# Kernel optimization log

Hardware: AMD Instinct MI355X
Metric: run time of the kernel (lower is better)

The kernel has to match this reference:

```python
import jax, jax.numpy as jnp
import numpy as np

R, DIL = 3, 2  # radius, dilation for neighbor correlation


def conv2d(x, w, b):
    # standard 3x3 stride-1 SAME conv, NCHW / OIHW
    y = jax.lax.conv_general_dilated(x, w, (1, 1), 'SAME',
                                     dimension_numbers=('NCHW', 'OIHW', 'NCHW'))
    return y + b[None, :, None, None]


def bilinear_gather(x, py, px):
    # x: (n,c,h,w); py/px: (n,K,h,w) float sampling coords; zero outside bounds
    n, c, h, w = x.shape
    y0 = jnp.floor(py); x0 = jnp.floor(px)
    wy = py - y0; wx = px - x0
    xf = x.reshape(n, c, h * w)

    def gather(yi, xi):
        valid = ((yi >= 0) & (yi < h) & (xi >= 0) & (xi < w)).astype(x.dtype)
        yc = jnp.clip(yi, 0, h - 1).astype(jnp.int32)
        xc = jnp.clip(xi, 0, w - 1).astype(jnp.int32)
        idx = (yc * w + xc).reshape(n, -1)  # (n, K*h*w)
        v = jax.vmap(lambda f, i: f[:, i])(xf, idx)  # (n, c, K*h*w)
        return v.reshape(n, c, *yi.shape[1:]) * valid[:, None]

    v00 = gather(y0, x0); v01 = gather(y0, x0 + 1)
    v10 = gather(y0 + 1, x0); v11 = gather(y0 + 1, x0 + 1)
    wy_ = wy[:, None]; wx_ = wx[:, None]
    return (v00 * (1 - wy_) * (1 - wx_) + v01 * (1 - wy_) * wx_
            + v10 * wy_ * (1 - wx_) + v11 * wy_ * wx_)


def dcn(x, w, b, ow, ob):
    # DCNv2-style modulated deformable 3x3 conv, stride 1, pad 1, 1 deformable group.
    # Offset/mask predicted by an internal conv: channels = [dy(9), dx(9), mask(9)].
    n, c, h, w_ = x.shape
    K = 9
    om = conv2d(x, ow, ob)  # (n, 27, h, w)
    dy, dx = om[:, :K], om[:, K:2 * K]
    mask = jax.nn.sigmoid(om[:, 2 * K:])
    ky, kx = jnp.meshgrid(jnp.arange(-1, 2), jnp.arange(-1, 2), indexing='ij')
    ky = ky.reshape(K).astype(x.dtype); kx = kx.reshape(K).astype(x.dtype)
    yy = jnp.arange(h, dtype=x.dtype)[None, None, :, None]
    xx = jnp.arange(w_, dtype=x.dtype)[None, None, None, :]
    py = yy + ky[None, :, None, None] + dy  # (n,K,h,w)
    px = xx + kx[None, :, None, None] + dx
    samp = bilinear_gather(x, py, px) * mask[:, None]  # (n,c,K,h,w)
    return jnp.einsum('nckhw,ock->nohw', samp, w.reshape(w.shape[0], c, K)) + b[None, :, None, None]


def ncf(f1, f2, radius, dilation):
    # neighbor_correlation_filter: unfold-based sliding-window dot-product attention
    n, c, h, w = f2.shape
    k = 2 * radius + 1
    pad = (k - 1) * dilation // 2
    f2p = jnp.pad(f2, ((0, 0), (0, 0), (pad, pad), (pad, pad)))
    # (n,c,K,h,w), tap order (ky outer, kx inner) matching F.unfold row-major layout
    patches = jnp.stack([f2p[:, :, i * dilation:i * dilation + h, j * dilation:j * dilation + w]
                         for i in range(k) for j in range(k)], axis=2)
    corr = jnp.einsum('nchw,nckhw->nkhw', f1, patches) / jnp.sqrt(jnp.asarray(c, f1.dtype))
    attn = jax.nn.softmax(corr, axis=1)
    sample = jnp.einsum('nkhw,nckhw->nchw', attn, patches)
    return sample, corr


def stargru(x, t, zw, zb, zow, zob, hw, hb, how, hob):
    tx = jnp.concatenate([x, t], axis=1)
    z = jax.nn.sigmoid(dcn(tx, zw, zb, zow, zob))
    r, _ = ncf(t, x, R, DIL)
    xt = jnp.tanh(dcn(jnp.concatenate([r, t], axis=1), hw, hb, how, hob))
    return (1.0 - z) * t + z * xt


def setup_inputs():
    key = jax.random.key(0)
    N, CIN, CH, H, W = 2, 256, 64, 96, 96
    ks = iter(jax.random.split(key, 32))

    def rn(shape, s=0.05):
        return jax.random.normal(next(ks), shape, jnp.float32) * s

    inp = {
        'x': jax.random.normal(next(ks), (N, CIN, H, W), jnp.float32),
        'template': jax.random.normal(next(ks), (N, CH, H, W), jnp.float32),
        'w_in': rn((CH, CIN, 3, 3)), 'b_in': jnp.zeros((CH,), jnp.float32),
        'w_out': rn((CIN, CH, 3, 3)), 'b_out': jnp.zeros((CIN,), jnp.float32),
    }
    for pre in ('enh_z', 'enh_h', 'upd_z', 'upd_h'):
        inp[pre + '_w'] = rn((CH, 2 * CH, 3, 3))
        inp[pre + '_b'] = jnp.zeros((CH,), jnp.float32)
        inp[pre + '_ow'] = rn((27, 2 * CH, 3, 3), 0.01)  # offset/mask conv (small init)
        inp[pre + '_ob'] = jnp.zeros((27,), jnp.float32)
    return inp


def reference(x, template, w_in, b_in, w_out, b_out,
              enh_z_w, enh_z_b, enh_z_ow, enh_z_ob,
              enh_h_w, enh_h_b, enh_h_ow, enh_h_ob,
              upd_z_w, upd_z_b, upd_z_ow, upd_z_ob,
              upd_h_w, upd_h_b, upd_h_ow, upd_h_ob):
    # CrossUpdate forward, post-first-frame branch (self.template is not None)
    xh = conv2d(x, w_in, b_in)
    x_enh = stargru(template, xh,
                    enh_z_w, enh_z_b, enh_z_ow, enh_z_ob,
                    enh_h_w, enh_h_b, enh_h_ow, enh_h_ob)
    new_template = stargru(xh, template,
                           upd_z_w, upd_z_b, upd_z_ow, upd_z_ob,
                           upd_h_w, upd_h_b, upd_h_ow, upd_h_ob)
    out = conv2d(x_enh, w_out, b_out)
    return (out, new_template)
```

## Files before the change

kernel.cpp:

```cpp
#include <hip/hip_runtime.h>
#include <hip/hip_bf16.h>

typedef __hip_bfloat16 bf16;
typedef unsigned short u16;
typedef unsigned int u32;
typedef __attribute__((ext_vector_type(8))) short short8;
typedef __attribute__((ext_vector_type(4))) short bh4;
typedef __attribute__((ext_vector_type(4))) float floatx4;

constexpr int N_ = 2, H_ = 96, W_ = 96, HW_ = H_ * W_;
constexpr int CIN_ = 256, CH_ = 64, C2_ = 128;

__device__ __forceinline__ float sigm(float v) { return 1.0f / (1.0f + __expf(-v)); }
__device__ __forceinline__ short f2b(float v) { bf16 h = __float2bfloat16(v); return *reinterpret_cast<short*>(&h); }
__device__ __forceinline__ float b2f(short s) {
    union { u32 i; float f; } v; v.i = ((u32)(u16)s) << 16; return v.f;
}

constexpr int A_IN_OFF = 0,                         A_IN_SZ  = 64 * 2304;
constexpr int A_OUT_OFF = A_IN_OFF + A_IN_SZ,       A_OUT_SZ = 256 * 576;
constexpr int A_OFF_OFF = A_OUT_OFF + A_OUT_SZ,     A_OFF_SZ = 64 * 1152;
constexpr int A_DCN_OFF = A_OFF_OFF + 4 * A_OFF_SZ, A_DCN_SZ = 64 * 1152;
constexpr int A_TOT = A_DCN_OFF + 4 * A_DCN_SZ;
constexpr int CVT_BLKS = A_TOT / 256;
constexpr int PREP_BLKS = 2880;

__global__ __launch_bounds__(256) void wprep(
        const float* __restrict__ w_in, const float* __restrict__ w_out,
        const float* __restrict__ ow0, const float* __restrict__ ow1,
        const float* __restrict__ ow2, const float* __restrict__ ow3,
        const float* __restrict__ w0, const float* __restrict__ w1,
        const float* __restrict__ w2, const float* __restrict__ w3,
        u16* __restrict__ dst,
        const float* __restrict__ x, const float* __restrict__ tpl,
        u16* __restrict__ xT, u16* __restrict__ ta, u16* __restrict__ tb) {
    if (blockIdx.x < CVT_BLKS) {
        int id = blockIdx.x * 256 + threadIdx.x;
        float v;
        if (id < A_OUT_OFF) {
            int l = id; int m = l / 2304, k = l % 2304; int tap = k >> 8, ic = k & 255;
            v = w_in[m * 2304 + ic * 9 + tap];
        } else if (id < A_OFF_OFF) {
            int l = id - A_OUT_OFF; int m = l / 576, k = l % 576; int tap = k / 64, ic = k & 63;
            v = w_out[m * 576 + ic * 9 + tap];
        } else if (id < A_DCN_OFF) {
            int l = id - A_OFF_OFF; int i = l / A_OFF_SZ, l2 = l % A_OFF_SZ;
            int m = l2 / 1152, k = l2 % 1152; int tap = k >> 7, ic = k & 127;
            const float* s = (i == 0) ? ow0 : (i == 1) ? ow1 : (i == 2) ? ow2 : ow3;
            v = (m < 27) ? s[m * 1152 + ic * 9 + tap] : 0.f;
        } else {
            int l = id - A_DCN_OFF; int i = l / A_DCN_SZ, l2 = l % A_DCN_SZ;
            int m = l2 / 1152, k = l2 % 1152; int tap = k >> 7, c = k & 127;
            const float* s = (i == 0) ? w0 : (i == 1) ? w1 : (i == 2) ? w2 : w3;
            v = s[m * 1152 + c * 9 + tap];
        }
        short sb = f2b(v);
        dst[id] = *reinterpret_cast<u16*>(&sb);
    } else {
        int id = (blockIdx.x - CVT_BLKS) * 256 + threadIdx.x;
        constexpr int XIDS = N_ * HW_ * 32;
        if (id < XIDS) {
            int c8 = id & 31;
            int pix = id >> 5;
            int n = pix / HW_, p = pix % HW_;
            const float* s = x + ((size_t)n * 256 + c8 * 8) * HW_ + p;
            short8 vv;
#pragma unroll
            for (int j = 0; j < 8; ++j) vv[j] = f2b(s[(size_t)j * HW_]);
            *reinterpret_cast<short8*>(xT + (size_t)pix * 256 + c8 * 8) = vv;
        } else {
            int id2 = id - XIDS;
            int c8 = id2 & 7;
            int pix = id2 >> 3;
            int n = pix / HW_, p = pix % HW_;
            const float* s = tpl + ((size_t)n * 64 + c8 * 8) * HW_ + p;
            short8 vv;
#pragma unroll
            for (int j = 0; j < 8; ++j) vv[j] = f2b(s[(size_t)j * HW_]);
            *reinterpret_cast<short8*>(ta + (size_t)pix * 128 + c8 * 8) = vv;
            *reinterpret_cast<short8*>(tb + (size_t)pix * 128 + 64 + c8 * 8) = vv;
        }
    }
}

template <int IC, int OCST, int CC>
__device__ __forceinline__ void conv_core(const u16* __restrict__ X,
                                          const u16* __restrict__ A,
                                          const float* __restrict__ bias,
                                          float* __restrict__ out,
                                          u16* __restrict__ ta, u16* __restrict__ tb,
                                          int r, int mt, int t) {
    constexpr int K = IC * 9;
    constexpr int ICC = IC / 64;
    __shared__ __align__(16) u16 Xl[3][50][72];
    int n = r / 192;
    int rr = r % 192;
    int y = rr >> 1, px0 = (rr & 1) * 48;
    int w = t >> 6, lane = t & 63, lm = lane & 15, q = lane >> 4;
    const u16* Arow = A + (size_t)(mt * 64 + w * 16 + lm) * K + q * 8;
    floatx4 acc[3];
#pragma unroll
    for (int a = 0; a < 3; ++a) acc[a] = {0.f, 0.f, 0.f, 0.f};
    const short8 zz = {0, 0, 0, 0, 0, 0, 0, 0};

    for (int icc = 0; icc < ICC; ++icc) {
        short8 af[9][2];
#pragma unroll
        for (int tap = 0; tap < 9; ++tap)
#pragma unroll
            for (int ks = 0; ks < 2; ++ks)
                af[tap][ks] = *reinterpret_cast<const short8*>(Arow + tap * IC + icc * 64 + ks * 32);
        __syncthreads();
#pragma unroll
        for (int it = 0; it < 5; ++it) {
            int id = it * 256 + t;
            if (id < 1200) {
                int ch8 = id & 7;
                int tmp = id >> 3;
                int pxl = tmp % 50, row = tmp / 50;
                int xg = px0 - 1 + pxl;
                int yg = y - 1 + row;
                bool vld = (yg >= 0) && (yg < 96) && (xg >= 0) && (xg < 96);
                short8 vv = zz;
                if (vld)
                    vv = *reinterpret_cast<const short8*>(
                        X + ((size_t)(n * HW_ + yg * 96 + xg)) * IC + icc * 64 + ch8 * 8);
                *reinterpret_cast<short8*>(&Xl[row][pxl][ch8 * 8]) = vv;
            }
        }
        __syncthreads();
#pragma unroll
        for (int tap = 0; tap < 9; ++tap) {
            int ky = tap / 3, kx = tap % 3;
#pragma unroll
            for (int ks = 0; ks < 2; ++ks) {
#pragma unroll
                for (int nf = 0; nf < 3; ++nf) {
                    short8 bv = *reinterpret_cast<const short8*>(&Xl[ky][nf * 16 + lm + kx][ks * 32 + q * 8]);
                    acc[nf] = __builtin_amdgcn_mfma_f32_16x16x32_bf16(af[tap][ks], bv, acc[nf], 0, 0, 0);
                }
            }
        }
    }
    int ocb = mt * 64 + w * 16 + q * 4;
#pragma unroll
    for (int nf = 0; nf < 3; ++nf) {
        int px = px0 + nf * 16 + lm;
        if constexpr (CC) {
            int pix = n * HW_ + y * 96 + px;
            bh4 bo;
#pragma unroll
            for (int rr2 = 0; rr2 < 4; ++rr2) {
                int oc = ocb + rr2;
                float v = acc[nf][rr2] + bias[oc];
                out[((size_t)(n * OCST + oc)) * HW_ + y * 96 + px] = v;
                bo[rr2] = f2b(v);
            }
            *reinterpret_cast<bh4*>(ta + (size_t)pix * 128 + 64 + ocb) = bo;
            *reinterpret_cast<bh4*>(tb + (size_t)pix * 128 + ocb) = bo;
        } else {
#pragma unroll
            for (int rr2 = 0; rr2 < 4; ++rr2) {
                int oc = ocb + rr2;
                if (oc < OCST)
                    out[((size_t)(n * OCST + oc)) * HW_ + y * 96 + px] = acc[nf][rr2] + bias[oc];
            }
        }
    }
}

template <int IC, int OCST, int CC>
__global__ __launch_bounds__(256) void conv_gemm(const u16* __restrict__ X,
                                                 const u16* __restrict__ A,
                                                 const float* __restrict__ bias,
                                                 float* __restrict__ out,
                                                 u16* __restrict__ ta, u16* __restrict__ tb) {
    int cpx = gridDim.x >> 3;
    int b = (blockIdx.x & 7) * cpx + (blockIdx.x >> 3);
    conv_core<IC, OCST, CC>(X, A, bias, out, ta, tb, b % 384, b / 384, threadIdx.x);
}

constexpr int P1XL_B = 21600;
constexpr int P1_B   = 26784;
constexpr int SM_SZ2 = 35424;

template <int GATE>
__device__ __forceinline__ void od_body(char* smem, int b, int t,
        const u16* __restrict__ X0, const u16* __restrict__ X1,
        const u16* __restrict__ Ao0, const u16* __restrict__ Ao1,
        const float* __restrict__ bo0, const float* __restrict__ bo1,
        const u16* __restrict__ Ad0, const u16* __restrict__ Ad1,
        const float* __restrict__ bd0, const float* __restrict__ bd1,
        float* __restrict__ o0, float* __restrict__ o1,
        const float* __restrict__ g0, const float* __restrict__ g1,
        const float* __restrict__ t0, const float* __restrict__ t1,
        u16* __restrict__ xeh, float* __restrict__ ontpl) {
    u16 (*Xl)[50][72] = reinterpret_cast<u16(*)[50][72]>(smem);
    float (*om_l)[48] = reinterpret_cast<float(*)[48]>(smem + P1XL_B);
    u16 (*Bl)[48][136] = reinterpret_cast<u16(*)[48][136]>(smem);
    int* s_y0 = reinterpret_cast<int*>(smem + P1_B);
    int* s_x0 = s_y0 + 432;
    float* s_wy = reinterpret_cast<float*>(s_x0 + 432);
    float* s_wx = s_wy + 432;
    float* s_m  = s_wx + 432;

    int inst = b / 384, r = b % 384;
    const u16* X = inst ? X1 : X0;
    const u16* Ao = inst ? Ao1 : Ao0;
    const float* bo = inst ? bo1 : bo0;
    const u16* Ad = inst ? Ad1 : Ad0;
    const float* bd = inst ? bd1 : bd0;
    int n = r / 192, rr = r % 192;
    int y = rr >> 1, px0 = (rr & 1) * 48;
    int w = t >> 6, lane = t & 63, lm = lane & 15, q = lane >> 4;
    const short8 zz = {0, 0, 0, 0, 0, 0, 0, 0};

    {
        const u16* Arow = Ao + (size_t)(w * 16 + lm) * 1152 + q * 8;
        floatx4 acc[3];
#pragma unroll
        for (int a = 0; a < 3; ++a) acc[a] = {0.f, 0.f, 0.f, 0.f};
        for (int icc = 0; icc < 2; ++icc) {
            short8 af[9][2];
#pragma unroll
            for (int tap = 0; tap < 9; ++tap)
#pragma unroll
                for (int ks = 0; ks < 2; ++ks)
                    af[tap][ks] = *reinterpret_cast<const short8*>(Arow + tap * 128 + icc * 64 + ks * 32);
            __syncthreads();
#pragma unroll
            for (int it = 0; it < 5; ++it) {
                int id = it * 256 + t;
                if (id < 1200) {
                    int ch8 = id & 7;
                    int tmp = id >> 3;
                    int pxl = tmp % 50, row = tmp / 50;
                    int xg = px0 - 1 + pxl;
                    int yg = y - 1 + row;
                    bool vld = (yg >= 0) && (yg < 96) && (xg >= 0) && (xg < 96);
                    short8 vv = zz;
                    if (vld)
                        vv = *reinterpret_cast<const short8*>(
                            X + ((size_t)(n * HW_ + yg * 96 + xg)) * 128 + icc * 64 + ch8 * 8);
                    *reinterpret_cast<short8*>(&Xl[row][pxl][ch8 * 8]) = vv;
                }
            }
            __syncthreads();
#pragma unroll
            for (int tap = 0; tap < 9; ++tap) {
                int ky = tap / 3, kx = tap % 3;
#pragma unroll
                for (int ks = 0; ks < 2; ++ks) {
#pragma unroll
                    for (int nf = 0; nf < 3; ++nf) {
                        short8 bv = *reinterpret_cast<const short8*>(&Xl[ky][nf * 16 + lm + kx][ks * 32 + q * 8]);
                        acc[nf] = __builtin_amdgcn_mfma_f32_16x16x32_bf16(af[tap][ks], bv, acc[nf], 0, 0, 0);
                    }
                }
            }
        }
        int ocb = w * 16 + q * 4;
#pragma unroll
        for (int nf = 0; nf < 3; ++nf) {
            int xl = nf * 16 + lm;
#pragma unroll
            for (int rr2 = 0; rr2 < 4; ++rr2) {
                int oc = ocb + rr2;
                if (oc < 27) om_l[oc][xl] = acc[nf][rr2] + bo[oc];
            }
        }
    }
    __syncthreads();

    for (int e = t; e < 432; e += 256) {
        int k9 = e / 48, xl = e % 48;
        int x = px0 + xl;
        float dy = om_l[k9][xl];
        float dx = om_l[9 + k9][xl];
        float ml = om_l[18 + k9][xl];
        float py = (float)y + (float)(k9 / 3 - 1) + dy;
        float px = (float)x + (float)(k9 % 3 - 1) + dx;
        float fy = floorf(py), fx = floorf(px);
        s_y0[e] = (int)fy; s_x0[e] = (int)fx;
        s_wy[e] = py - fy; s_wx[e] = px - fx; s_m[e] = sigm(ml);
    }
    __syncthreads();

    const u16* Arow = Ad + (size_t)(w * 16 + lm) * 1152 + q * 8;
    floatx4 acc[3];
#pragma unroll
    for (int a = 0; a < 3; ++a) acc[a] = {0.f, 0.f, 0.f, 0.f};
    const u16* txn = X + (size_t)n * HW_ * 128;
    int p = 0;
    int cg = t & 15, px0i = t >> 4;
    short8 cr[3][4];
    short8 afP[2][2];

    auto issueT = [&](int tap) {
#pragma unroll
        for (int s = 0; s < 3; ++s) {
            int pxi = px0i + s * 16;
            int ce = tap * 48 + pxi;
            int y0 = s_y0[ce], x0c = s_x0[ce];
            bool yv0 = (y0 >= 0) & (y0 < 96), yv1 = (y0 >= -1) & (y0 < 95);
            bool xv0 = (x0c >= 0) & (x0c < 96), xv1 = (x0c >= -1) & (x0c < 95);
            const u16* gb = txn + (long)(y0 * 96 + x0c) * 128 + cg * 8;
            cr[s][0] = (yv0 && xv0) ? *reinterpret_cast<const short8*>(gb) : zz;
            cr[s][1] = (yv0 && xv1) ? *reinterpret_cast<const short8*>(gb + 128) : zz;
            cr[s][2] = (yv1 && xv0) ? *reinterpret_cast<const short8*>(gb + 96 * 128) : zz;
            cr[s][3] = (yv1 && xv1) ? *reinterpret_cast<const short8*>(gb + 96 * 128 + 128) : zz;
        }
    };
    auto computeT = [&](int tap) {
#pragma unroll
        for (int s = 0; s < 3; ++s) {
            int pxi = px0i + s * 16;
            int ce = tap * 48 + pxi;
            float wy = s_wy[ce], wx = s_wx[ce], m = s_m[ce];
            float w00 = (1.f - wy) * (1.f - wx) * m;
            float w01 = (1.f - wy) * wx * m;
            float w10 = wy * (1.f - wx) * m;
            float w11 = wy * wx * m;
            short8 vv;
#pragma unroll
            for (int j = 0; j < 8; ++j) {
                float f = b2f(cr[s][0][j]) * w00 + b2f(cr[s][1][j]) * w01 +
                          b2f(cr[s][2][j]) * w10 + b2f(cr[s][3][j]) * w11;
                vv[j] = f2b(f);
            }
            *reinterpret_cast<short8*>(&Bl[p][pxi][cg * 8]) = vv;
        }
    };

    issueT(0);
    for (int tap = 0; tap < 9; ++tap) {
        if (tap > 0) {
#pragma unroll
            for (int half = 0; half < 2; ++half)
#pragma unroll
                for (int ks = 0; ks < 2; ++ks)
#pragma unroll
                    for (int nf = 0; nf < 3; ++nf) {
                        short8 bv = *reinterpret_cast<const short8*>(
                            &Bl[p ^ 1][nf * 16 + lm][half * 64 + ks * 32 + q * 8]);
                        acc[nf] = __builtin_amdgcn_mfma_f32_16x16x32_bf16(afP[half][ks], bv, acc[nf], 0, 0, 0);
                    }
        }
        computeT(tap);
        if (tap < 8) issueT(tap + 1);
#pragma unroll
        for (int half = 0; half < 2; ++half)
#pragma unroll
            for (int ks = 0; ks < 2; ++ks)
                afP[half][ks] = *reinterpret_cast<const short8*>(Arow + (tap * 2 + half) * 64 + ks * 32);
        __syncthreads();
        p ^= 1;
    }
#pragma unroll
    for (int half = 0; half < 2; ++half)
#pragma unroll
        for (int ks = 0; ks < 2; ++ks)
#pragma unroll
            for (int nf = 0; nf < 3; ++nf) {
                short8 bv = *reinterpret_cast<const short8*>(
                    &Bl[p ^ 1][nf * 16 + lm][half * 64 + ks * 32 + q * 8]);
                acc[nf] = __builtin_amdgcn_mfma_f32_16x16x32_bf16(afP[half][ks], bv, acc[nf], 0, 0, 0);
            }

    int ocb = w * 16 + q * 4;
    if constexpr (GATE == 0) {
        float* out = inst ? o1 : o0;
#pragma unroll
        for (int nf = 0; nf < 3; ++nf) {
            int px = px0 + nf * 16 + lm;
#pragma unroll
            for (int rr2 = 0; rr2 < 4; ++rr2) {
                int oc = ocb + rr2;
                out[((size_t)(n * CH_ + oc)) * HW_ + y * 96 + px] = acc[nf][rr2] + bd[oc];
            }
        }
    } else {
        const float* gz = inst ? g1 : g0;
        const float* tt = inst ? t1 : t0;
#pragma unroll
        for (int nf = 0; nf < 3; ++nf) {
            int px = px0 + nf * 16 + lm;
            if (!inst) {
                bh4 bo4;
#pragma unroll
                for (int rr2 = 0; rr2 < 4; ++rr2) {
                    int oc = ocb + rr2;
                    size_t idx = ((size_t)(n * CH_ + oc)) * HW_ + y * 96 + px;
                    float z = sigm(gz[idx]);
                    float xt = tanhf(acc[nf][rr2] + bd[oc]);
                    bo4[rr2] = f2b((1.f - z) * tt[idx] + z * xt);
                }
                *reinterpret_cast<bh4*>(xeh + ((size_t)(n * HW_ + y * 96 + px)) * 64 + ocb) = bo4;
            } else {
#pragma unroll
                for (int rr2 = 0; rr2 < 4; ++rr2) {
                    int oc = ocb + rr2;
                    size_t idx = ((size_t)(n * CH_ + oc)) * HW_ + y * 96 + px;
                    float z = sigm(gz[idx]);
                    float xt = tanhf(acc[nf][rr2] + bd[oc]);
                    ontpl[idx] = (1.f - z) * tt[idx] + z * xt;
                }
            }
        }
    }
}

__device__ __forceinline__ void ncf_body(char* smem, int b, int t,
        const u16* __restrict__ in0, const u16* __restrict__ in1,
        u16* __restrict__ out0, u16* __restrict__ out1) {
    u16 (*sF2)[28][72] = reinterpret_cast<u16(*)[28][72]>(smem);
    u16 (*sF1)[72] = reinterpret_cast<u16(*)[72]>(smem + 28224);
    float (*sc)[52] = reinterpret_cast<float(*)[52]>(smem + 30528);
    int inst = b / 1152, bb = b % 1152;
    const u16* txh = inst ? in1 : in0;
    u16* txh2 = inst ? out1 : out0;
    int n = bb / 576, rem = bb % 576;
    int y = rem / 6, x0 = (rem % 6) * 16;
    const u16* base = txh + (size_t)n * HW_ * 128;
    const short8 zz = {0, 0, 0, 0, 0, 0, 0, 0};

    for (int id = t; id < 1568; id += 256) {
        int ch8 = id & 7;
        int tmp = id >> 3;
        int px = tmp % 28, row = tmp / 28;
        int yy = y + row * 2 - 6;
        int xg = x0 - 6 + px;
        short8 vv = zz;
        if (yy >= 0 && yy < 96 && xg >= 0 && xg < 96)
            vv = *reinterpret_cast<const short8*>(base + (size_t)(yy * 96 + xg) * 128 + ch8 * 8);
        *reinterpret_cast<short8*>(&sF2[row][px][ch8 * 8]) = vv;
    }
    if (t < 128) {
        int ch8 = t & 7, lp0 = t >> 3;
        short8 vv = *reinterpret_cast<const short8*>(base + (size_t)(y * 96 + x0 + lp0) * 128 + 64 + ch8 * 8);
        *reinterpret_cast<short8*>(&sF1[lp0][ch8 * 8]) = vv;
    }
    __syncthreads();

    int lp = t >> 4, j = t & 15;
    for (int k = j; k < 49; k += 16) {
        int ky = k / 7, kx = k % 7;
        const u16* f2p = &sF2[ky][lp + 2 * kx][0];
        const u16* f1p = &sF1[lp][0];
        float s = 0.f;
#pragma unroll
        for (int c8 = 0; c8 < 8; ++c8) {
            short8 a = *reinterpret_cast<const short8*>(f1p + c8 * 8);
            short8 b2 = *reinterpret_cast<const short8*>(f2p + c8 * 8);
#pragma unroll
            for (int u = 0; u < 8; ++u) s += b2f(a[u]) * b2f(b2[u]);
        }
        sc[lp][k] = s * 0.125f;
    }
    float mx = -1e30f;
    for (int k = j; k < 49; k += 16) mx = fmaxf(mx, sc[lp][k]);
#pragma unroll
    for (int m = 1; m <= 8; m <<= 1) mx = fmaxf(mx, __shfl_xor(mx, m, 64));
    float e[4];
    float sum = 0.f;
    int cnt = 0;
    for (int k = j; k < 49; k += 16) { e[cnt] = __expf(sc[lp][k] - mx); sum += e[cnt]; ++cnt; }
#pragma unroll
    for (int m = 1; m <= 8; m <<= 1) sum += __shfl_xor(sum, m, 64);
    float inv = 1.f / sum;
    cnt = 0;
    for (int k = j; k < 49; k += 16) sc[lp][k] = e[cnt++] * inv;
    __syncthreads();
    int ch0 = j * 4;
    float acc[4];
#pragma unroll
    for (int u = 0; u < 4; ++u) acc[u] = 0.f;
#pragma unroll
    for (int k = 0; k < 49; ++k) {
        int ky = k / 7, kx = k % 7;
        float a = sc[lp][k];
        bh4 f2 = *reinterpret_cast<const bh4*>(&sF2[ky][lp + 2 * kx][ch0]);
#pragma unroll
        for (int u = 0; u < 4; ++u) acc[u] += a * b2f(f2[u]);
    }
    int p = y * 96 + x0 + lp;
    u16* obase = txh2 + (size_t)n * HW_ * 128 + (size_t)p * 128;
    bh4 ro;
#pragma unroll
    for (int u = 0; u < 4; ++u) ro[u] = f2b(acc[u]);
    *reinterpret_cast<bh4*>(obase + ch0) = ro;
    *reinterpret_cast<bh4*>(obase + 64 + ch0) =
        *reinterpret_cast<const bh4*>(&sF1[lp][ch0]);
}

__global__ __launch_bounds__(256, 4) void od0_ncf(
        const u16* __restrict__ Xa, const u16* __restrict__ Xb,
        const u16* __restrict__ Ao0, const u16* __restrict__ Ao1,
        const float* __restrict__ bo0, const float* __restrict__ bo1,
        const u16* __restrict__ Ad0, const u16* __restrict__ Ad1,
        const float* __restrict__ bd0, const float* __restrict__ bd1,
        float* __restrict__ dz0, float* __restrict__ dz1,
        u16* __restrict__ t2a, u16* __restrict__ t2b) {
    __shared__ __align__(16) char smem[SM_SZ2];
    int t = threadIdx.x;
    if (blockIdx.x < 768) {
        int bid = blockIdx.x;
        int b = (bid & 7) * 96 + (bid >> 3);
        od_body<0>(smem, b, t, Xa, Xb, Ao0, Ao1, bo0, bo1, Ad0, Ad1, bd0, bd1,
                   dz0, dz1, nullptr, nullptr, nullptr, nullptr, nullptr, nullptr);
    } else {
        int bid = blockIdx.x - 768;
        int b = (bid & 7) * 288 + (bid >> 3);
        ncf_body(smem, b, t, Xa, Xb, t2a, t2b);
    }
}

__global__ __launch_bounds__(256, 4) void od_gate(
        const u16* __restrict__ Xa, const u16* __restrict__ Xb,
        const u16* __restrict__ Ao0, const u16* __restrict__ Ao1,
        const float* __restrict__ bo0, const float* __restrict__ bo1,
        const u16* __restrict__ Ad0, const u16* __restrict__ Ad1,
        const float* __restrict__ bd0, const float* __restrict__ bd1,
        const float* __restrict__ g0, const float* __restrict__ g1,
        const float* __restrict__ t0, const float* __restrict__ t1,
        u16* __restrict__ xeh, float* __restrict__ ontpl) {
    __shared__ __align__(16) char smem[SM_SZ2];
    int bid = blockIdx.x;
    int b = (bid & 7) * 96 + (bid >> 3);
    od_body<1>(smem, b, threadIdx.x, Xa, Xb, Ao0, Ao1, bo0, bo1, Ad0, Ad1, bd0, bd1,
               nullptr, nullptr, g0, g1, t0, t1, xeh, ontpl);
}

extern "C" void kernel_launch(void* const* d_in, const int* in_sizes, int n_in,
                              void* d_out, int out_size, void* d_ws, size_t ws_size,
                              hipStream_t stream) {
    const float* x     = (const float*)d_in[0];
    const float* tpl   = (const float*)d_in[1];
    const float* w_in  = (const float*)d_in[2];
    const float* b_in  = (const float*)d_in[3];
    const float* w_out = (const float*)d_in[4];
    const float* b_out = (const float*)d_in[5];
    const float *pw[4], *pb[4], *pow_[4], *pob[4];
    for (int i = 0; i < 4; ++i) {
        pw[i]   = (const float*)d_in[6 + 4 * i];
        pb[i]   = (const float*)d_in[7 + 4 * i];
        pow_[i] = (const float*)d_in[8 + 4 * i];
        pob[i]  = (const float*)d_in[9 + 4 * i];
    }
    float* out_main = (float*)d_out;
    float* out_ntpl = out_main + (size_t)N_ * CIN_ * HW_;

    u16* Aws = (u16*)d_ws;
    u16* xT     = Aws + A_TOT;
    u16* txh_a  = xT + (size_t)N_ * HW_ * CIN_;
    u16* txh_b  = txh_a + (size_t)N_ * HW_ * C2_;
    u16* txh2_a = txh_b + (size_t)N_ * HW_ * C2_;
    u16* txh2_b = txh2_a + (size_t)N_ * HW_ * C2_;
    u16* xeh    = txh2_b + (size_t)N_ * HW_ * C2_;
    float* fws = (float*)(xeh + (size_t)N_ * HW_ * CH_);
    size_t off = 0;
    float* xh   = fws + off; off += (size_t)N_ * CH_ * HW_;
    float* dz_a = fws + off; off += (size_t)N_ * CH_ * HW_;
    float* dz_b = fws + off; off += (size_t)N_ * CH_ * HW_;

    wprep<<<CVT_BLKS + PREP_BLKS, 256, 0, stream>>>(
        w_in, w_out, pow_[0], pow_[1], pow_[2], pow_[3], pw[0], pw[1], pw[2], pw[3], Aws,
        x, tpl, xT, txh_a, txh_b);
    conv_gemm<CIN_, 64, 1><<<384, 256, 0, stream>>>(xT, Aws + A_IN_OFF, b_in, xh, txh_a, txh_b);

    od0_ncf<<<3072, 256, 0, stream>>>(txh_a, txh_b,
        Aws + A_OFF_OFF + 0 * A_OFF_SZ, Aws + A_OFF_OFF + 2 * A_OFF_SZ, pob[0], pob[2],
        Aws + A_DCN_OFF + 0 * A_DCN_SZ, Aws + A_DCN_OFF + 2 * A_DCN_SZ, pb[0], pb[2],
        dz_a, dz_b, txh2_a, txh2_b);

    od_gate<<<768, 256, 0, stream>>>(txh2_a, txh2_b,
        Aws + A_OFF_OFF + 1 * A_OFF_SZ, Aws + A_OFF_OFF + 3 * A_OFF_SZ, pob[1], pob[3],
        Aws + A_DCN_OFF + 1 * A_DCN_SZ, Aws + A_DCN_OFF + 3 * A_DCN_SZ, pb[1], pb[3],
        dz_a, dz_b, xh, tpl, xeh, out_ntpl);

    conv_gemm<CH_, 256, 0><<<1536, 256, 0, stream>>>(xeh, Aws + A_OUT_OFF, b_out, out_main, nullptr, nullptr);
}
```

Before: 298.0 us.

## Split offset+deformable conv into independent per-wave 16-pixel strips without block barriers

```diff
diff --git a/kernel.cpp b/kernel.cpp
--- a/kernel.cpp
+++ b/kernel.cpp
@@ -180,12 +180,11 @@
     conv_core<IC, OCST, CC>(X, A, bias, out, ta, tb, b % 384, b / 384, threadIdx.x);
 }
 
-constexpr int P1XL_B = 21600;
-constexpr int P1_B   = 26784;
-constexpr int SM_SZ2 = 35424;
+constexpr int ODW_B = 9504;
+constexpr int SM_FAT = 4 * ODW_B;
 
 template <int GATE>
-__device__ __forceinline__ void od_body(char* smem, int b, int t,
+__device__ __forceinline__ void od_wave(char* lds, int strip, int lane,
         const u16* __restrict__ X0, const u16* __restrict__ X1,
         const u16* __restrict__ Ao0, const u16* __restrict__ Ao1,
         const float* __restrict__ bo0, const float* __restrict__ bo1,
@@ -195,85 +194,65 @@
         const float* __restrict__ g0, const float* __restrict__ g1,
         const float* __restrict__ t0, const float* __restrict__ t1,
         u16* __restrict__ xeh, float* __restrict__ ontpl) {
-    u16 (*Xl)[50][72] = reinterpret_cast<u16(*)[50][72]>(smem);
-    float (*om_l)[48] = reinterpret_cast<float(*)[48]>(smem + P1XL_B);
-    u16 (*Bl)[48][136] = reinterpret_cast<u16(*)[48][136]>(smem);
-    int* s_y0 = reinterpret_cast<int*>(smem + P1_B);
-    int* s_x0 = s_y0 + 432;
-    float* s_wy = reinterpret_cast<float*>(s_x0 + 432);
-    float* s_wx = s_wy + 432;
-    float* s_m  = s_wx + 432;
-
-    int inst = b / 384, r = b % 384;
+    u16 (*Xl)[18][72] = reinterpret_cast<u16(*)[18][72]>(lds);
+    float (*om_l)[16] = reinterpret_cast<float(*)[16]>(lds + 7776);
+    int* s_y0 = reinterpret_cast<int*>(lds);
+    int* s_x0 = s_y0 + 144;
+    float* s_wy = reinterpret_cast<float*>(s_x0 + 144);
+    float* s_wx = s_wy + 144;
+    float* s_m  = s_wx + 144;
+
+    int inst = strip / 1152, rem = strip % 1152;
+    int n = rem / 576, rr = rem % 576;
+    int y = rr / 6, px0 = (rr % 6) * 16;
     const u16* X = inst ? X1 : X0;
     const u16* Ao = inst ? Ao1 : Ao0;
     const float* bo = inst ? bo1 : bo0;
     const u16* Ad = inst ? Ad1 : Ad0;
     const float* bd = inst ? bd1 : bd0;
-    int n = r / 192, rr = r % 192;
-    int y = rr >> 1, px0 = (rr & 1) * 48;
-    int w = t >> 6, lane = t & 63, lm = lane & 15, q = lane >> 4;
+    int lm = lane & 15, q = lane >> 4;
     const short8 zz = {0, 0, 0, 0, 0, 0, 0, 0};
 
-    {
-        const u16* Arow = Ao + (size_t)(w * 16 + lm) * 1152 + q * 8;
-        floatx4 acc[3];
-#pragma unroll
-        for (int a = 0; a < 3; ++a) acc[a] = {0.f, 0.f, 0.f, 0.f};
-        for (int icc = 0; icc < 2; ++icc) {
-            short8 af[9][2];
-#pragma unroll
-            for (int tap = 0; tap < 9; ++tap)
-#pragma unroll
-                for (int ks = 0; ks < 2; ++ks)
-                    af[tap][ks] = *reinterpret_cast<const short8*>(Arow + tap * 128 + icc * 64 + ks * 32);
-            __syncthreads();
-#pragma unroll
-            for (int it = 0; it < 5; ++it) {
-                int id = it * 256 + t;
-                if (id < 1200) {
-                    int ch8 = id & 7;
-                    int tmp = id >> 3;
-                    int pxl = tmp % 50, row = tmp / 50;
-                    int xg = px0 - 1 + pxl;
-                    int yg = y - 1 + row;
-                    bool vld = (yg >= 0) && (yg < 96) && (xg >= 0) && (xg < 96);
-                    short8 vv = zz;
-                    if (vld)
-                        vv = *reinterpret_cast<const short8*>(
-                            X + ((size_t)(n * HW_ + yg * 96 + xg)) * 128 + icc * 64 + ch8 * 8);
-                    *reinterpret_cast<short8*>(&Xl[row][pxl][ch8 * 8]) = vv;
+    floatx4 accO[2];
+    accO[0] = {0.f, 0.f, 0.f, 0.f};
+    accO[1] = {0.f, 0.f, 0.f, 0.f};
+    for (int icc = 0; icc < 2; ++icc) {
+        for (int id = lane; id < 432; id += 64) {
+            int ch8 = id & 7;
+            int tmp = id >> 3;
+            int pxl = tmp % 18, row = tmp / 18;
+            int xg = px0 - 1 + pxl, yg = y - 1 + row;
+            short8 vv = zz;
+            if (yg >= 0 && yg < 96 && xg >= 0 && xg < 96)
+                vv = *reinterpret_cast<const short8*>(
+                    X + ((size_t)(n * HW_ + yg * 96 + xg)) * 128 + icc * 64 + ch8 * 8);
+            *reinterpret_cast<short8*>(&Xl[row][pxl][ch8 * 8]) = vv;
+        }
+#pragma unroll
+        for (int tap = 0; tap < 9; ++tap) {
+            int ky = tap / 3, kx = tap % 3;
+#pragma unroll
+            for (int ks = 0; ks < 2; ++ks) {
+                short8 bv = *reinterpret_cast<const short8*>(&Xl[ky][lm + kx][ks * 32 + q * 8]);
+#pragma unroll
+                for (int mt = 0; mt < 2; ++mt) {
+                    short8 af = *reinterpret_cast<const short8*>(
+                        Ao + (size_t)(mt * 16 + lm) * 1152 + tap * 128 + icc * 64 + ks * 32 + q * 8);
+                    accO[mt] = __builtin_amdgcn_mfma_f32_16x16x32_bf16(af, bv, accO[mt], 0, 0, 0);
                 }
             }
-            __syncthreads();
-#pragma unroll
-            for (int tap = 0; tap < 9; ++tap) {
-                int ky = tap / 3, kx = tap % 3;
-#pragma unroll
-                for (int ks = 0; ks < 2; ++ks) {
-#pragma unroll
-                    for (int nf = 0; nf < 3; ++nf) {
-                        short8 bv = *reinterpret_cast<const short8*>(&Xl[ky][nf * 16 + lm + kx][ks * 32 + q * 8]);
-                        acc[nf] = __builtin_amdgcn_mfma_f32_16x16x32_bf16(af[tap][ks], bv, acc[nf], 0, 0, 0);
-                    }
-                }
-            }
-        }
-        int ocb = w * 16 + q * 4;
-#pragma unroll
-        for (int nf = 0; nf < 3; ++nf) {
-            int xl = nf * 16 + lm;
-#pragma unroll
-            for (int rr2 = 0; rr2 < 4; ++rr2) {
-                int oc = ocb + rr2;
-                if (oc < 27) om_l[oc][xl] = acc[nf][rr2] + bo[oc];
-            }
-        }
-    }
-    __syncthreads();
-
-    for (int e = t; e < 432; e += 256) {
-        int k9 = e / 48, xl = e % 48;
+        }
+    }
+#pragma unroll
+    for (int mt = 0; mt < 2; ++mt)
+#pragma unroll
+        for (int rr2 = 0; rr2 < 4; ++rr2) {
+            int oc = mt * 16 + q * 4 + rr2;
+            if (oc < 27) om_l[oc][lm] = accO[mt][rr2] + bo[oc];
+        }
+
+    for (int e = lane; e < 144; e += 64) {
+        int k9 = e >> 4, xl = e & 15;
         int x = px0 + xl;
         float dy = om_l[k9][xl];
         float dx = om_l[9 + k9][xl];
@@ -284,128 +263,94 @@
         s_y0[e] = (int)fy; s_x0[e] = (int)fx;
         s_wy[e] = py - fy; s_wx[e] = px - fx; s_m[e] = sigm(ml);
     }
-    __syncthreads();
-
-    const u16* Arow = Ad + (size_t)(w * 16 + lm) * 1152 + q * 8;
-    floatx4 acc[3];
-#pragma unroll
-    for (int a = 0; a < 3; ++a) acc[a] = {0.f, 0.f, 0.f, 0.f};
+
+    floatx4 acc[4];
+#pragma unroll
+    for (int a = 0; a < 4; ++a) acc[a] = {0.f, 0.f, 0.f, 0.f};
     const u16* txn = X + (size_t)n * HW_ * 128;
-    int p = 0;
-    int cg = t & 15, px0i = t >> 4;
-    short8 cr[3][4];
-    short8 afP[2][2];
-
-    auto issueT = [&](int tap) {
-#pragma unroll
-        for (int s = 0; s < 3; ++s) {
-            int pxi = px0i + s * 16;
-            int ce = tap * 48 + pxi;
-            int y0 = s_y0[ce], x0c = s_x0[ce];
-            bool yv0 = (y0 >= 0) & (y0 < 96), yv1 = (y0 >= -1) & (y0 < 95);
-            bool xv0 = (x0c >= 0) & (x0c < 96), xv1 = (x0c >= -1) & (x0c < 95);
-            const u16* gb = txn + (long)(y0 * 96 + x0c) * 128 + cg * 8;
-            cr[s][0] = (yv0 && xv0) ? *reinterpret_cast<const short8*>(gb) : zz;
-            cr[s][1] = (yv0 && xv1) ? *reinterpret_cast<const short8*>(gb + 128) : zz;
-            cr[s][2] = (yv1 && xv0) ? *reinterpret_cast<const short8*>(gb + 96 * 128) : zz;
-            cr[s][3] = (yv1 && xv1) ? *reinterpret_cast<const short8*>(gb + 96 * 128 + 128) : zz;
-        }
-    };
-    auto computeT = [&](int tap) {
-#pragma unroll
-        for (int s = 0; s < 3; ++s) {
-            int pxi = px0i + s * 16;
-            int ce = tap * 48 + pxi;
-            float wy = s_wy[ce], wx = s_wx[ce], m = s_m[ce];
-            float w00 = (1.f - wy) * (1.f - wx) * m;
-            float w01 = (1.f - wy) * wx * m;
-            float w10 = wy * (1.f - wx) * m;
-            float w11 = wy * wx * m;
-            short8 vv;
-#pragma unroll
-            for (int j = 0; j < 8; ++j) {
-                float f = b2f(cr[s][0][j]) * w00 + b2f(cr[s][1][j]) * w01 +
-                          b2f(cr[s][2][j]) * w10 + b2f(cr[s][3][j]) * w11;
-                vv[j] = f2b(f);
-            }
-            *reinterpret_cast<short8*>(&Bl[p][pxi][cg * 8]) = vv;
-        }
-    };
-
-    issueT(0);
     for (int tap = 0; tap < 9; ++tap) {
-        if (tap > 0) {
-#pragma unroll
-            for (int half = 0; half < 2; ++half)
-#pragma unroll
-                for (int ks = 0; ks < 2; ++ks)
-#pragma unroll
-                    for (int nf = 0; nf < 3; ++nf) {
-                        short8 bv = *reinterpret_cast<const short8*>(
-                            &Bl[p ^ 1][nf * 16 + lm][half * 64 + ks * 32 + q * 8]);
-                        acc[nf] = __builtin_amdgcn_mfma_f32_16x16x32_bf16(afP[half][ks], bv, acc[nf], 0, 0, 0);
-                    }
-        }
-        computeT(tap);
-        if (tap < 8) issueT(tap + 1);
-#pragma unroll
-        for (int half = 0; half < 2; ++half)
-#pragma unroll
-            for (int ks = 0; ks < 2; ++ks)
-                afP[half][ks] = *reinterpret_cast<const short8*>(Arow + (tap * 2 + half) * 64 + ks * 32);
-        __syncthreads();
-        p ^= 1;
-    }
-#pragma unroll
-    for (int half = 0; half < 2; ++half)
-#pragma unroll
-        for (int ks = 0; ks < 2; ++ks)
-#pragma unroll
-            for (int nf = 0; nf < 3; ++nf) {
-                short8 bv = *reinterpret_cast<const short8*>(
-                    &Bl[p ^ 1][nf * 16 + lm][half * 64 + ks * 32 + q * 8]);
-                acc[nf] = __builtin_amdgcn_mfma_f32_16x16x32_bf16(afP[half][ks], bv, acc[nf], 0, 0, 0);
-            }
-
-    int ocb = w * 16 + q * 4;
+        int ce = tap * 16 + lm;
+        int y0 = s_y0[ce], x0c = s_x0[ce];
+        float wy = s_wy[ce], wx = s_wx[ce], m = s_m[ce];
+        float w00 = (1.f - wy) * (1.f - wx) * m;
+        float w01 = (1.f - wy) * wx * m;
+        float w10 = wy * (1.f - wx) * m;
+        float w11 = wy * wx * m;
+        bool yv0 = (y0 >= 0) & (y0 < 96), yv1 = (y0 >= -1) & (y0 < 95);
+        bool xv0 = (x0c >= 0) & (x0c < 96), xv1 = (x0c >= -1) & (x0c < 95);
+        const u16* gb = txn + (long)(y0 * 96 + x0c) * 128 + q * 8;
+        short8 bf[4];
+#pragma unroll
+        for (int half = 0; half < 2; ++half) {
+            short8 c[2][4];
+#pragma unroll
+            for (int it = 0; it < 2; ++it) {
+                int choff = (half * 2 + it) * 32;
+                c[it][0] = (yv0 && xv0) ? *reinterpret_cast<const short8*>(gb + choff) : zz;
+                c[it][1] = (yv0 && xv1) ? *reinterpret_cast<const short8*>(gb + choff + 128) : zz;
+                c[it][2] = (yv1 && xv0) ? *reinterpret_cast<const short8*>(gb + choff + 96 * 128) : zz;
+                c[it][3] = (yv1 && xv1) ? *reinterpret_cast<const short8*>(gb + choff + 96 * 128 + 128) : zz;
+            }
+#pragma unroll
+            for (int it = 0; it < 2; ++it) {
+                short8 vv;
+#pragma unroll
+                for (int j = 0; j < 8; ++j) {
+                    float f = b2f(c[it][0][j]) * w00 + b2f(c[it][1][j]) * w01 +
+                              b2f(c[it][2][j]) * w10 + b2f(c[it][3][j]) * w11;
+                    vv[j] = f2b(f);
+                }
+                bf[half * 2 + it] = vv;
+            }
+        }
+#pragma unroll
+        for (int ks = 0; ks < 4; ++ks)
+#pragma unroll
+            for (int mt = 0; mt < 4; ++mt) {
+                short8 af = *reinterpret_cast<const short8*>(
+                    Ad + (size_t)(mt * 16 + lm) * 1152 + tap * 128 + ks * 32 + q * 8);
+                acc[mt] = __builtin_amdgcn_mfma_f32_16x16x32_bf16(af, bf[ks], acc[mt], 0, 0, 0);
+            }
+    }
+
+    int px = px0 + lm;
     if constexpr (GATE == 0) {
         float* out = inst ? o1 : o0;
 #pragma unroll
-        for (int nf = 0; nf < 3; ++nf) {
-            int px = px0 + nf * 16 + lm;
+        for (int mt = 0; mt < 4; ++mt)
 #pragma unroll
             for (int rr2 = 0; rr2 < 4; ++rr2) {
-                int oc = ocb + rr2;
-                out[((size_t)(n * CH_ + oc)) * HW_ + y * 96 + px] = acc[nf][rr2] + bd[oc];
-            }
-        }
+                int oc = mt * 16 + q * 4 + rr2;
+                out[((size_t)(n * CH_ + oc)) * HW_ + y * 96 + px] = acc[mt][rr2] + bd[oc];
+            }
     } else {
         const float* gz = inst ? g1 : g0;
         const float* tt = inst ? t1 : t0;
-#pragma unroll
-        for (int nf = 0; nf < 3; ++nf) {
-            int px = px0 + nf * 16 + lm;
-            if (!inst) {
+        if (!inst) {
+#pragma unroll
+            for (int mt = 0; mt < 4; ++mt) {
                 bh4 bo4;
 #pragma unroll
                 for (int rr2 = 0; rr2 < 4; ++rr2) {
-                    int oc = ocb + rr2;
+                    int oc = mt * 16 + q * 4 + rr2;
                     size_t idx = ((size_t)(n * CH_ + oc)) * HW_ + y * 96 + px;
                     float z = sigm(gz[idx]);
-                    float xt = tanhf(acc[nf][rr2] + bd[oc]);
+                    float xt = tanhf(acc[mt][rr2] + bd[oc]);
                     bo4[rr2] = f2b((1.f - z) * tt[idx] + z * xt);
                 }
-                *reinterpret_cast<bh4*>(xeh + ((size_t)(n * HW_ + y * 96 + px)) * 64 + ocb) = bo4;
-            } else {
+                *reinterpret_cast<bh4*>(xeh + ((size_t)(n * HW_ + y * 96 + px)) * 64 + mt * 16 + q * 4) = bo4;
+            }
+        } else {
+#pragma unroll
+            for (int mt = 0; mt < 4; ++mt)
 #pragma unroll
                 for (int rr2 = 0; rr2 < 4; ++rr2) {
-                    int oc = ocb + rr2;
+                    int oc = mt * 16 + q * 4 + rr2;
                     size_t idx = ((size_t)(n * CH_ + oc)) * HW_ + y * 96 + px;
                     float z = sigm(gz[idx]);
-                    float xt = tanhf(acc[nf][rr2] + bd[oc]);
+                    float xt = tanhf(acc[mt][rr2] + bd[oc]);
                     ontpl[idx] = (1.f - z) * tt[idx] + z * xt;
                 }
-            }
         }
     }
 }
@@ -501,15 +446,17 @@
         const float* __restrict__ bd0, const float* __restrict__ bd1,
         float* __restrict__ dz0, float* __restrict__ dz1,
         u16* __restrict__ t2a, u16* __restrict__ t2b) {
-    __shared__ __align__(16) char smem[SM_SZ2];
+    __shared__ __align__(16) char smem[SM_FAT];
     int t = threadIdx.x;
-    if (blockIdx.x < 768) {
+    if (blockIdx.x < 576) {
         int bid = blockIdx.x;
-        int b = (bid & 7) * 96 + (bid >> 3);
-        od_body<0>(smem, b, t, Xa, Xb, Ao0, Ao1, bo0, bo1, Ad0, Ad1, bd0, bd1,
-                   dz0, dz1, nullptr, nullptr, nullptr, nullptr, nullptr, nullptr);
+        int b = (bid & 7) * 72 + (bid >> 3);
+        int wid = t >> 6, lane = t & 63;
+        od_wave<0>(smem + wid * ODW_B, b * 4 + wid, lane, Xa, Xb, Ao0, Ao1, bo0, bo1,
+                   Ad0, Ad1, bd0, bd1, dz0, dz1,
+                   nullptr, nullptr, nullptr, nullptr, nullptr, nullptr);
     } else {
-        int bid = blockIdx.x - 768;
+        int bid = blockIdx.x - 576;
         int b = (bid & 7) * 288 + (bid >> 3);
         ncf_body(smem, b, t, Xa, Xb, t2a, t2b);
     }
@@ -524,11 +471,12 @@
         const float* __restrict__ g0, const float* __restrict__ g1,
         const float* __restrict__ t0, const float* __restrict__ t1,
         u16* __restrict__ xeh, float* __restrict__ ontpl) {
-    __shared__ __align__(16) char smem[SM_SZ2];
+    __shared__ __align__(16) char smem[SM_FAT];
     int bid = blockIdx.x;
-    int b = (bid & 7) * 96 + (bid >> 3);
-    od_body<1>(smem, b, threadIdx.x, Xa, Xb, Ao0, Ao1, bo0, bo1, Ad0, Ad1, bd0, bd1,
-               nullptr, nullptr, g0, g1, t0, t1, xeh, ontpl);
+    int b = (bid & 7) * 72 + (bid >> 3);
+    int wid = threadIdx.x >> 6, lane = threadIdx.x & 63;
+    od_wave<1>(smem + wid * ODW_B, b * 4 + wid, lane, Xa, Xb, Ao0, Ao1, bo0, bo1,
+               Ad0, Ad1, bd0, bd1, nullptr, nullptr, g0, g1, t0, t1, xeh, ontpl);
 }
 
 extern "C" void kernel_launch(void* const* d_in, const int* in_sizes, int n_in,
@@ -568,12 +516,12 @@
         x, tpl, xT, txh_a, txh_b);
     conv_gemm<CIN_, 64, 1><<<384, 256, 0, stream>>>(xT, Aws + A_IN_OFF, b_in, xh, txh_a, txh_b);
 
-    od0_ncf<<<3072, 256, 0, stream>>>(txh_a, txh_b,
+    od0_ncf<<<2880, 256, 0, stream>>>(txh_a, txh_b,
         Aws + A_OFF_OFF + 0 * A_OFF_SZ, Aws + A_OFF_OFF + 2 * A_OFF_SZ, pob[0], pob[2],
         Aws + A_DCN_OFF + 0 * A_DCN_SZ, Aws + A_DCN_OFF + 2 * A_DCN_SZ, pb[0], pb[2],
         dz_a, dz_b, txh2_a, txh2_b);
 
-    od_gate<<<768, 256, 0, stream>>>(txh2_a, txh2_b,
+    od_gate<<<576, 256, 0, stream>>>(txh2_a, txh2_b,
         Aws + A_OFF_OFF + 1 * A_OFF_SZ, Aws + A_OFF_OFF + 3 * A_OFF_SZ, pob[1], pob[3],
         Aws + A_DCN_OFF + 1 * A_DCN_SZ, Aws + A_DCN_OFF + 3 * A_DCN_SZ, pb[1], pb[3],
         dz_a, dz_b, xh, tpl, xeh, out_ntpl);
```

Measured after the change: 436.6 us. +46.5%, slower.

## Split weight prep and fuse input conv with remaining conversions, double-buffered

Applied to the files above, without the earlier changes.

```diff
diff --git a/kernel.cpp b/kernel.cpp
--- a/kernel.cpp
+++ b/kernel.cpp
@@ -22,25 +22,125 @@
 constexpr int A_OFF_OFF = A_OUT_OFF + A_OUT_SZ,     A_OFF_SZ = 64 * 1152;
 constexpr int A_DCN_OFF = A_OFF_OFF + 4 * A_OFF_SZ, A_DCN_SZ = 64 * 1152;
 constexpr int A_TOT = A_DCN_OFF + 4 * A_DCN_SZ;
-constexpr int CVT_BLKS = A_TOT / 256;
-constexpr int PREP_BLKS = 2880;
-
-__global__ __launch_bounds__(256) void wprep(
-        const float* __restrict__ w_in, const float* __restrict__ w_out,
+
+constexpr int WPA_X = 2304;
+constexpr int WPA_AIN = A_IN_SZ / 256;
+__global__ __launch_bounds__(256) void wprep_a(
+        const float* __restrict__ x, const float* __restrict__ w_in,
+        u16* __restrict__ xT, u16* __restrict__ dst) {
+    if (blockIdx.x < WPA_X) {
+        int id = blockIdx.x * 256 + threadIdx.x;
+        int c8 = id & 31;
+        int pix = id >> 5;
+        int n = pix / HW_, p = pix % HW_;
+        const float* s = x + ((size_t)n * 256 + c8 * 8) * HW_ + p;
+        short8 vv;
+#pragma unroll
+        for (int j = 0; j < 8; ++j) vv[j] = f2b(s[(size_t)j * HW_]);
+        *reinterpret_cast<short8*>(xT + (size_t)pix * 256 + c8 * 8) = vv;
+    } else {
+        int id = (blockIdx.x - WPA_X) * 256 + threadIdx.x;
+        int m = id / 2304, k = id % 2304;
+        int tap = k >> 8, ic = k & 255;
+        short sb = f2b(w_in[m * 2304 + ic * 9 + tap]);
+        dst[id] = *reinterpret_cast<u16*>(&sb);
+    }
+}
+
+constexpr int CF_CONV = 384;
+constexpr int CF_WREST = (A_TOT - A_IN_SZ) / 256;
+constexpr int CF_TPL = N_ * HW_ * 8 / 256;
+constexpr int CF_GRID = CF_CONV + CF_WREST + CF_TPL;
+
+__global__ __launch_bounds__(256) void cin_fat(
+        const u16* __restrict__ X, const u16* __restrict__ A,
+        const float* __restrict__ bias, float* __restrict__ out,
+        u16* __restrict__ ta, u16* __restrict__ tb,
+        const float* __restrict__ w_out,
         const float* __restrict__ ow0, const float* __restrict__ ow1,
         const float* __restrict__ ow2, const float* __restrict__ ow3,
         const float* __restrict__ w0, const float* __restrict__ w1,
         const float* __restrict__ w2, const float* __restrict__ w3,
-        u16* __restrict__ dst,
-        const float* __restrict__ x, const float* __restrict__ tpl,
-        u16* __restrict__ xT, u16* __restrict__ ta, u16* __restrict__ tb) {
-    if (blockIdx.x < CVT_BLKS) {
-        int id = blockIdx.x * 256 + threadIdx.x;
+        u16* __restrict__ dst, const float* __restrict__ tpl) {
+    __shared__ __align__(16) u16 Xl[2][3][50][72];
+    int t = threadIdx.x;
+    if (blockIdx.x < CF_CONV) {
+        int bid = blockIdx.x;
+        int b = (bid & 7) * 48 + (bid >> 3);
+        int n = b / 192, rr = b % 192;
+        int y = rr >> 1, px0 = (rr & 1) * 48;
+        int w = t >> 6, lane = t & 63, lm = lane & 15, q = lane >> 4;
+        const u16* Arow = A + (size_t)(w * 16 + lm) * 2304 + q * 8;
+        floatx4 acc[3];
+#pragma unroll
+        for (int a = 0; a < 3; ++a) acc[a] = {0.f, 0.f, 0.f, 0.f};
+        const short8 zz = {0, 0, 0, 0, 0, 0, 0, 0};
+
+        auto stage = [&](int icc, int pb) {
+#pragma unroll
+            for (int it = 0; it < 5; ++it) {
+                int id = it * 256 + t;
+                if (id < 1200) {
+                    int ch8 = id & 7;
+                    int tmp = id >> 3;
+                    int pxl = tmp % 50, row = tmp / 50;
+                    int xg = px0 - 1 + pxl;
+                    int yg = y - 1 + row;
+                    bool vld = (yg >= 0) && (yg < 96) && (xg >= 0) && (xg < 96);
+                    short8 vv = zz;
+                    if (vld)
+                        vv = *reinterpret_cast<const short8*>(
+                            X + ((size_t)(n * HW_ + yg * 96 + xg)) * 256 + icc * 64 + ch8 * 8);
+                    *reinterpret_cast<short8*>(&Xl[pb][row][pxl][ch8 * 8]) = vv;
+                }
+            }
+        };
+
+        stage(0, 0);
+        __syncthreads();
+#pragma unroll
+        for (int icc = 0; icc < 4; ++icc) {
+            const int pb = icc & 1;
+            if (icc < 3) stage(icc + 1, pb ^ 1);
+            short8 af[9][2];
+#pragma unroll
+            for (int tap = 0; tap < 9; ++tap)
+#pragma unroll
+                for (int ks = 0; ks < 2; ++ks)
+                    af[tap][ks] = *reinterpret_cast<const short8*>(Arow + tap * 256 + icc * 64 + ks * 32);
+#pragma unroll
+            for (int tap = 0; tap < 9; ++tap) {
+                int ky = tap / 3, kx = tap % 3;
+#pragma unroll
+                for (int ks = 0; ks < 2; ++ks)
+#pragma unroll
+                    for (int nf = 0; nf < 3; ++nf) {
+                        short8 bv = *reinterpret_cast<const short8*>(&Xl[pb][ky][nf * 16 + lm + kx][ks * 32 + q * 8]);
+                        acc[nf] = __builtin_amdgcn_mfma_f32_16x16x32_bf16(af[tap][ks], bv, acc[nf], 0, 0, 0);
+                    }
+            }
+            __syncthreads();
+        }
+        int ocb = w * 16 + q * 4;
+#pragma unroll
+        for (int nf = 0; nf < 3; ++nf) {
+            int px = px0 + nf * 16 + lm;
+            int pix = n * HW_ + y * 96 + px;
+            bh4 bo;
+#pragma unroll
+            for (int rr2 = 0; rr2 < 4; ++rr2) {
+                int oc = ocb + rr2;
+                float v = acc[nf][rr2] + bias[oc];
+                out[((size_t)(n * 64 + oc)) * HW_ + y * 96 + px] = v;
+                bo[rr2] = f2b(v);
+            }
+            *reinterpret_cast<bh4*>(ta + (size_t)pix * 128 + 64 + ocb) = bo;
+            *reinterpret_cast<bh4*>(tb + (size_t)pix * 128 + ocb) = bo;
+        }
+    } else if (blockIdx.x < CF_CONV + CF_WREST) {
+        int id = A_IN_SZ + (blockIdx.x - CF_CONV) * 256 + t;
         float v;
-        if (id < A_OUT_OFF) {
-            int l = id; int m = l / 2304, k = l % 2304; int tap = k >> 8, ic = k & 255;
-            v = w_in[m * 2304 + ic * 9 + tap];
-        } else if (id < A_OFF_OFF) {
+        if (id < A_OFF_OFF) {
             int l = id - A_OUT_OFF; int m = l / 576, k = l % 576; int tap = k / 64, ic = k & 63;
             v = w_out[m * 576 + ic * 9 + tap];
         } else if (id < A_DCN_OFF) {
@@ -57,42 +157,30 @@
         short sb = f2b(v);
         dst[id] = *reinterpret_cast<u16*>(&sb);
     } else {
-        int id = (blockIdx.x - CVT_BLKS) * 256 + threadIdx.x;
-        constexpr int XIDS = N_ * HW_ * 32;
-        if (id < XIDS) {
-            int c8 = id & 31;
-            int pix = id >> 5;
-            int n = pix / HW_, p = pix % HW_;
-            const float* s = x + ((size_t)n * 256 + c8 * 8) * HW_ + p;
-            short8 vv;
-#pragma unroll
-            for (int j = 0; j < 8; ++j) vv[j] = f2b(s[(size_t)j * HW_]);
-            *reinterpret_cast<short8*>(xT + (size_t)pix * 256 + c8 * 8) = vv;
-        } else {
-            int id2 = id - XIDS;
-            int c8 = id2 & 7;
-            int pix = id2 >> 3;
-            int n = pix / HW_, p = pix % HW_;
-            const float* s = tpl + ((size_t)n * 64 + c8 * 8) * HW_ + p;
-            short8 vv;
-#pragma unroll
-            for (int j = 0; j < 8; ++j) vv[j] = f2b(s[(size_t)j * HW_]);
-            *reinterpret_cast<short8*>(ta + (size_t)pix * 128 + c8 * 8) = vv;
-            *reinterpret_cast<short8*>(tb + (size_t)pix * 128 + 64 + c8 * 8) = vv;
-        }
-    }
-}
-
-template <int IC, int OCST, int CC>
-__device__ __forceinline__ void conv_core(const u16* __restrict__ X,
-                                          const u16* __restrict__ A,
-                                          const float* __restrict__ bias,
-                                          float* __restrict__ out,
-                                          u16* __restrict__ ta, u16* __restrict__ tb,
-                                          int r, int mt, int t) {
+        int id2 = (blockIdx.x - CF_CONV - CF_WREST) * 256 + t;
+        int c8 = id2 & 7;
+        int pix = id2 >> 3;
+        int n = pix / HW_, p = pix % HW_;
+        const float* s = tpl + ((size_t)n * 64 + c8 * 8) * HW_ + p;
+        short8 vv;
+#pragma unroll
+        for (int j = 0; j < 8; ++j) vv[j] = f2b(s[(size_t)j * HW_]);
+        *reinterpret_cast<short8*>(ta + (size_t)pix * 128 + c8 * 8) = vv;
+        *reinterpret_cast<short8*>(tb + (size_t)pix * 128 + 64 + c8 * 8) = vv;
+    }
+}
+
+template <int IC, int OCST>
+__global__ __launch_bounds__(256) void conv_gemm(const u16* __restrict__ X,
+                                                 const u16* __restrict__ A,
+                                                 const float* __restrict__ bias,
+                                                 float* __restrict__ out) {
+    __shared__ __align__(16) u16 Xl[3][50][72];
+    int cpx = gridDim.x >> 3;
+    int bb = (blockIdx.x & 7) * cpx + (blockIdx.x >> 3);
+    int r = bb % 384, mt = bb / 384, t = threadIdx.x;
     constexpr int K = IC * 9;
     constexpr int ICC = IC / 64;
-    __shared__ __align__(16) u16 Xl[3][50][72];
     int n = r / 192;
     int rr = r % 192;
     int y = rr >> 1, px0 = (rr & 1) * 48;
@@ -146,38 +234,13 @@
 #pragma unroll
     for (int nf = 0; nf < 3; ++nf) {
         int px = px0 + nf * 16 + lm;
-        if constexpr (CC) {
-            int pix = n * HW_ + y * 96 + px;
-            bh4 bo;
-#pragma unroll
-            for (int rr2 = 0; rr2 < 4; ++rr2) {
-                int oc = ocb + rr2;
-                float v = acc[nf][rr2] + bias[oc];
-                out[((size_t)(n * OCST + oc)) * HW_ + y * 96 + px] = v;
-                bo[rr2] = f2b(v);
-            }
-            *reinterpret_cast<bh4*>(ta + (size_t)pix * 128 + 64 + ocb) = bo;
-            *reinterpret_cast<bh4*>(tb + (size_t)pix * 128 + ocb) = bo;
-        } else {
-#pragma unroll
-            for (int rr2 = 0; rr2 < 4; ++rr2) {
-                int oc = ocb + rr2;
-                if (oc < OCST)
-                    out[((size_t)(n * OCST + oc)) * HW_ + y * 96 + px] = acc[nf][rr2] + bias[oc];
-            }
-        }
-    }
-}
-
-template <int IC, int OCST, int CC>
-__global__ __launch_bounds__(256) void conv_gemm(const u16* __restrict__ X,
-                                                 const u16* __restrict__ A,
-                                                 const float* __restrict__ bias,
-                                                 float* __restrict__ out,
-                                                 u16* __restrict__ ta, u16* __restrict__ tb) {
-    int cpx = gridDim.x >> 3;
-    int b = (blockIdx.x & 7) * cpx + (blockIdx.x >> 3);
-    conv_core<IC, OCST, CC>(X, A, bias, out, ta, tb, b % 384, b / 384, threadIdx.x);
+#pragma unroll
+        for (int rr2 = 0; rr2 < 4; ++rr2) {
+            int oc = ocb + rr2;
+            if (oc < OCST)
+                out[((size_t)(n * OCST + oc)) * HW_ + y * 96 + px] = acc[nf][rr2] + bias[oc];
+        }
+    }
 }
 
 constexpr int P1XL_B = 21600;
@@ -563,20 +626,16 @@
     float* dz_a = fws + off; off += (size_t)N_ * CH_ * HW_;
     float* dz_b = fws + off; off += (size_t)N_ * CH_ * HW_;
 
-    wprep<<<CVT_BLKS + PREP_BLKS, 256, 0, stream>>>(
-        w_in, w_out, pow_[0], pow_[1], pow_[2], pow_[3], pw[0], pw[1], pw[2], pw[3], Aws,
-        x, tpl, xT, txh_a, txh_b);
-    conv_gemm<CIN_, 64, 1><<<384, 256, 0, stream>>>(xT, Aws + A_IN_OFF, b_in, xh, txh_a, txh_b);
-
+    wprep_a<<<WPA_X + WPA_AIN, 256, 0, stream>>>(x, w_in, xT, Aws);
+    cin_fat<<<CF_GRID, 256, 0, stream>>>(xT, Aws + A_IN_OFF, b_in, xh, txh_a, txh_b,
+        w_out, pow_[0], pow_[1], pow_[2], pow_[3], pw[0], pw[1], pw[2], pw[3], Aws, tpl);
     od0_ncf<<<3072, 256, 0, stream>>>(txh_a, txh_b,
         Aws + A_OFF_OFF + 0 * A_OFF_SZ, Aws + A_OFF_OFF + 2 * A_OFF_SZ, pob[0], pob[2],
         Aws + A_DCN_OFF + 0 * A_DCN_SZ, Aws + A_DCN_OFF + 2 * A_DCN_SZ, pb[0], pb[2],
         dz_a, dz_b, txh2_a, txh2_b);
-
     od_gate<<<768, 256, 0, stream>>>(txh2_a, txh2_b,
         Aws + A_OFF_OFF + 1 * A_OFF_SZ, Aws + A_OFF_OFF + 3 * A_OFF_SZ, pob[1], pob[3],
         Aws + A_DCN_OFF + 1 * A_DCN_SZ, Aws + A_DCN_OFF + 3 * A_DCN_SZ, pb[1], pb[3],
         dz_a, dz_b, xh, tpl, xeh, out_ntpl);
-
-    conv_gemm<CH_, 256, 0><<<1536, 256, 0, stream>>>(xeh, Aws + A_OUT_OFF, b_out, out_main, nullptr, nullptr);
-}
+    conv_gemm<CH_, 256><<<1536, 256, 0, stream>>>(xeh, Aws + A_OUT_OFF, b_out, out_main);
+}
```

Result: no change. 292.9 us, median of 3 (-1.7%).
